# Kernel optimization log

Measured on AMD Instinct MI355X. Metric: run time of the kernel, lower is better.

The kernel has to match this reference:

```python
import jax, jax.numpy as jnp
import numpy as np

# ---- constants mirroring the torch module ----
OSAMP = 8            # temporal oversampling factor
MAX_ITER = 10        # forward solver iterations (LBFGS replaced by fixed GD)
NEG_SHIFT = 2 * OSAMP
OTP = 5              # baseline frames subtracted from ctc/aif
C_SHARP = 500.0      # sharpness constant C=500 in fermi_ir_func
LR = 0.1             # fixed step size for the deterministic forward solve


def interp_linear_1d(x, size):
    # interp_linear_1D: linear upsampling along last (time) axis
    return jax.image.resize(x, x.shape[:-1] + (size,), method='linear')


def fermi_ir(eta, t_os):
    # eta: [B,3,H,W] = (amplitude A, decay rate k, delay t0); t_os: [Tos]
    tsh = t_os - t_os[NEG_SHIFT]                    # negative time shift
    A = eta[:, 0][..., None]                        # [B,H,W,1]
    k = eta[:, 1][..., None]
    t0 = eta[:, 2][..., None]
    step = jax.nn.sigmoid(C_SHARP * tsh)            # sharp causal onset (C=500)
    return A * jax.nn.sigmoid(k * (t0 - tsh)) * step  # [B,H,W,Tos]


def convolve(aif, ir):
    # linear convolution along time via FFT; output aligned with neg_shift offset
    Tos = ir.shape[-1]
    n = 2 * Tos
    Fa = jnp.fft.rfft(aif, n=n, axis=-1)            # [B,1,1,n/2+1]
    Fi = jnp.fft.rfft(ir, n=n, axis=-1)             # [B,H,W,n/2+1]
    full = jnp.fft.irfft(Fa * Fi, n=n, axis=-1)
    return jax.lax.dynamic_slice_in_dim(full, NEG_SHIFT, Tos, axis=-1)


def make_objective(ctc, aif, time, eta_prior, lambda_reg):
    # preprocessing from FermiDataConsLBFGS.forward
    aif = aif - aif[..., :OTP].mean(-1, keepdims=True)
    ctc = ctc - ctc[..., :OTP].mean(-1, keepdims=True)
    Tos = OSAMP * ctc.shape[-1]
    aif_os = interp_linear_1d(aif, Tos)
    ctc_os = interp_linear_1d(ctc, Tos)
    t_os = interp_linear_1d(time, Tos)
    ctc_dc = ctc_os[..., ::OSAMP]                   # [B,H,W,T]
    C_nn = (eta_prior ** 2).sum(axis=(0, 2, 3), keepdims=True)  # [1,3,1,1]
    C_dc = (ctc_dc ** 2).sum()
    sp_lam = jax.nn.softplus(lambda_reg).squeeze()

    def F_obj(eta):  # FermiDConsObj.__call__ (OD disabled: indx_dc = all frames)
        ir = fermi_ir(eta, t_os)
        ctc_est = convolve(aif_os, ir)[..., ::OSAMP] / OSAMP
        dc = ((ctc_dc - ctc_est) ** 2 / C_dc).sum()
        reg = sp_lam * (((eta - eta_prior) ** 2) / C_nn).sum()
        pos = (jax.nn.relu(-eta) ** 2).sum()
        return dc + reg + pos
    return F_obj


def setup_inputs():
    key = jax.random.key(0)
    k1, k2, k3, k4 = jax.random.split(key, 4)
    B, H, W, T = 1, 128, 128, 64
    ctc = jax.random.normal(k1, (B, H, W, T), jnp.float32) * 0.1
    aif = jax.random.uniform(k2, (B, 1, 1, T), jnp.float32)
    time = jnp.arange(T, dtype=jnp.float32)
    seg = jnp.ones((B, H, W), jnp.int32)
    eta_nn = jax.random.uniform(k3, (B, 3, H, W), jnp.float32)
    lambda_reg = jax.random.normal(k4, (1,), jnp.float32)
    return {"ctc": ctc, "aif": aif, "time": time, "seg": seg,
            "eta_nn": eta_nn, "lambda_reg": lambda_reg}


def reference(ctc, aif, time, seg, eta_nn, lambda_reg):
    # seg only affects the (disabled) outlier-detection path
    F_obj = make_objective(ctc, aif, time, eta_nn, lambda_reg)
    gradF = jax.grad(F_obj)

    def step(eta, _):
        return eta - LR * gradF(eta), None

    eta_pi, _ = jax.lax.scan(step, eta_nn, None, length=MAX_ITER)
    return eta_pi
```

## Files before the change

kernel.cpp:

```cpp
#include <hip/hip_runtime.h>
#include <math.h>

#define T_IN 64
#define NPIX 16384
#define MAX_ITER 10
#define NSLOT 43
#define MAGIC 0x13579BDFu

typedef _Float16 half8_t __attribute__((ext_vector_type(8)));
typedef __fp16   fp16x2  __attribute__((ext_vector_type(2)));
typedef float    f32x4   __attribute__((ext_vector_type(4)));
typedef int      i32x4   __attribute__((ext_vector_type(4)));

union H8 { half8_t v; fp16x2 h2[4]; i32x4 i4; };

__device__ __forceinline__ float rcp_fast(float x) { return __builtin_amdgcn_rcpf(x); }

constexpr int NTMIN[16]   = {0,0,0,0,0,1,1,1,1,2,2,2,2,3,3,3};
constexpr int KTS[2][8]   = {{0,2,4,6,8,10,12,14},{1,3,5,7,9,11,13,15}};
constexpr int LBASE[2][8] = {{0,4,8,12,15,18,20,22},{0,4,8,11,14,16,18,19}};
constexpr int SLOTS[2][23] = {
  {0,1,2,3,8,9,10,11,16,17,18,19,23,24,25,29,30,31,34,35,38,39,41},
  {4,5,6,7,12,13,14,15,20,21,22,26,27,28,32,33,36,37,40,42,0,0,0}};

template<int P>
__device__ __forceinline__ void kloop(float K, float T0, int q,
        const float* tshs, const i32x4 (&Breg)[23], f32x4 (&acc)[3][4]) {
    float nK = -K;
    float r  = __expf(0.125f * K);
    #pragma unroll
    for (int i = 0; i < 8; ++i) {
        const int kt = KTS[P][i];
        f32x4 tv0 = *(const f32x4*)&tshs[32*kt + 8*q];
        f32x4 tv1 = *(const f32x4*)&tshs[32*kt + 8*q + 4];
        float d1[8];
        d1[0]=T0-tv0[0]; d1[1]=T0-tv0[1]; d1[2]=T0-tv0[2]; d1[3]=T0-tv0[3];
        d1[4]=T0-tv1[0]; d1[5]=T0-tv1[1]; d1[6]=T0-tv1[2]; d1[7]=T0-tv1[3];
        float x[8];
        if (kt == 0 || kt == 15) {
            bool edge = (kt == 0) ? (q == 0) : (q == 3);
            if (edge) {
                #pragma unroll
                for (int j = 0; j < 8; ++j) x[j] = __expf(nK * d1[j]);
            } else {
                x[0] = __expf(nK * d1[0]);
                #pragma unroll
                for (int j = 1; j < 8; ++j) x[j] = x[j-1] * r;
            }
        } else {
            x[0] = __expf(nK * d1[0]);
            #pragma unroll
            for (int j = 1; j < 8; ++j) x[j] = x[j-1] * r;
        }
        H8 F0h, F1h, F2h;
        #pragma unroll
        for (int jj = 0; jj < 4; ++jj) {
            float s1a = rcp_fast(1.0f + x[2*jj]);
            float s1b = rcp_fast(1.0f + x[2*jj+1]);
            fp16x2 sh  = (fp16x2){(__fp16)s1a, (__fp16)s1b};
            fp16x2 d1h = __builtin_amdgcn_cvt_pkrtz(d1[2*jj], d1[2*jj+1]);
            fp16x2 eh  = sh - sh*sh;
            F0h.h2[jj] = sh;
            F1h.h2[jj] = eh * d1h;
            F2h.h2[jj] = eh;
        }
        #pragma unroll
        for (int nt = NTMIN[kt]; nt < 4; ++nt) {
            int sl = LBASE[P][i] + nt - NTMIN[kt];
            H8 bh; bh.i4 = Breg[sl];
            acc[0][nt] = __builtin_amdgcn_mfma_f32_16x16x32_f16(F0h.v, bh.v, acc[0][nt], 0, 0, 0);
            acc[1][nt] = __builtin_amdgcn_mfma_f32_16x16x32_f16(F1h.v, bh.v, acc[1][nt], 0, 0, 0);
            acc[2][nt] = __builtin_amdgcn_mfma_f32_16x16x32_f16(F2h.v, bh.v, acc[2][nt], 0, 0, 0);
        }
    }
}

__global__ __launch_bounds__(512, 2) void k_all(
        const float* __restrict__ ctc,  const float* __restrict__ aif,
        const float* __restrict__ timev,const float* __restrict__ lam,
        const float* __restrict__ eta,  unsigned int* __restrict__ flags,
        f32x4* __restrict__ partials,   float* __restrict__ out) {
    __shared__ i32x4 Bs[NSLOT * 64];
    __shared__ f32x4 cbuf[4][64][12];
    __shared__ float ebuf[4][16][4];
    __shared__ float tshs[512];
    __shared__ float aifos[512];
    __shared__ float a_s[64], t_s[64];
    __shared__ f32x4 red[4];

    const int tid  = threadIdx.x;
    const int lane = tid & 63;
    const int wid  = tid >> 6;
    const int par  = wid & 1;
    const int pair = wid >> 1;
    const int q = lane >> 4, n = lane & 15;
    const int pixbase = blockIdx.x * 64 + pair * 16;
    const int mypix   = pixbase + n;

    if (tid < 64) { a_s[tid] = aif[tid]; t_s[tid] = timev[tid]; }
    float A  = eta[mypix];
    float K  = eta[NPIX + mypix];
    float T0 = eta[2*NPIX + mypix];
    const float pA = A, pK = K, pT = T0;
    __syncthreads();
    {
        float m5a = 0.2f * (a_s[0]+a_s[1]+a_s[2]+a_s[3]+a_s[4]);
        float t16;
        {
            float xx = 1.5625f; int i0 = (int)xx; float f = xx - (float)i0;
            t16 = t_s[i0]*(1.0f-f) + t_s[i0+1]*f;
        }
        int i = tid;
        float x = ((float)i - 3.5f) * 0.125f;
        float ao, to;
        if (x <= 0.0f)       { ao = a_s[0]  - m5a; to = t_s[0];  }
        else if (x >= 63.0f) { ao = a_s[63] - m5a; to = t_s[63]; }
        else {
            int i0 = (int)x; float f = x - (float)i0;
            ao = (a_s[i0]-m5a)*(1.0f-f) + (a_s[i0+1]-m5a)*f;
            to = t_s[i0]*(1.0f-f) + t_s[i0+1]*f;
        }
        aifos[i] = ao;
        tshs[i]  = to - t16;
    }

    float dcreg[4][4];
    if (par == 0) {
        #pragma unroll
        for (int reg = 0; reg < 4; ++reg) {
            const float* cp = ctc + (pixbase + q*4 + reg) * T_IN;
            float m5 = 0.2f * (cp[0]+cp[1]+cp[2]+cp[3]+cp[4]);
            #pragma unroll
            for (int nt = 0; nt < 4; ++nt) {
                int d = nt*16 + n;
                float cc = cp[d] - m5;
                float cm = cp[(d > 0) ? d-1 : 0] - m5;
                dcreg[nt][reg] = (d == 0) ? cc : (0.4375f*cm + 0.5625f*cc);
            }
        }
        float vs = 0.f;
        #pragma unroll
        for (int nt = 0; nt < 4; ++nt)
            #pragma unroll
            for (int r2 = 0; r2 < 4; ++r2) vs += dcreg[nt][r2]*dcreg[nt][r2];
        f32x4 pv = (f32x4){vs, 0.25f*A*A, 0.25f*K*K, 0.25f*T0*T0};
        #pragma unroll
        for (int m = 1; m < 64; m <<= 1) {
            pv.x += __shfl_xor(pv.x, m); pv.y += __shfl_xor(pv.y, m);
            pv.z += __shfl_xor(pv.z, m); pv.w += __shfl_xor(pv.w, m);
        }
        if (lane == 0) red[pair] = pv;
    }
    __syncthreads();
    if (tid == 0) {
        f32x4 s = red[0] + red[1] + red[2] + red[3];
        partials[blockIdx.x] = s;
        __threadfence();
        __hip_atomic_store(&flags[blockIdx.x], MAGIC, __ATOMIC_RELEASE,
                           __HIP_MEMORY_SCOPE_AGENT);
    }

    for (int idx = tid; idx < NSLOT * 64; idx += 512) {
        int slot = idx >> 6, l = idx & 63;
        int kt, nt;
        if (slot < 20)      { kt = slot >> 2; nt = slot & 3; }
        else if (slot < 32) { int s = slot - 20; int d3 = s / 3; kt = 5 + d3; nt = 1 + (s - 3*d3); }
        else if (slot < 40) { int s = slot - 32; kt = 9 + (s >> 1); nt = 2 + (s & 1); }
        else                { kt = 13 + (slot - 40); nt = 3; }
        int kbase = 32*kt + 8*(l >> 4);
        int m = 16 + 8 * (16*nt + (l & 15));
        H8 bh;
        #pragma unroll
        for (int jj = 0; jj < 4; ++jj) {
            float v[2];
            #pragma unroll
            for (int h = 0; h < 2; ++h) {
                int k  = kbase + 2*jj + h;
                int ai = m - k;
                float s2 = 1.0f / (1.0f + __expf(-500.0f * tshs[k]));
                v[h] = (ai >= 0 && ai < 512) ? s2 * aifos[ai] * 0.125f : 0.0f;
            }
            bh.h2[jj] = (fp16x2){(__fp16)v[0], (__fp16)v[1]};
        }
        Bs[idx] = bh.i4;
    }
    __syncthreads();

    i32x4 Breg[23];
    if (par == 0) {
        #pragma unroll
        for (int s = 0; s < 23; ++s) Breg[s] = Bs[SLOTS[0][s]*64 + lane];
    } else {
        #pragma unroll
        for (int s = 0; s < 20; ++s) Breg[s] = Bs[SLOTS[1][s]*64 + lane];
    }

    if (tid < 256)
        while (__hip_atomic_load(&flags[tid], __ATOMIC_ACQUIRE,
                                 __HIP_MEMORY_SCOPE_AGENT) != MAGIC)
            __builtin_amdgcn_s_sleep(2);
    __syncthreads();

    f32x4 tot = partials[lane] + partials[64+lane] + partials[128+lane]
              + partials[192+lane];
    #pragma unroll
    for (int m = 1; m < 64; m <<= 1) {
        tot.x += __shfl_xor(tot.x, m); tot.y += __shfl_xor(tot.y, m);
        tot.z += __shfl_xor(tot.z, m); tot.w += __shfl_xor(tot.w, m);
    }
    float spl;
    {
        float xl = lam[0];
        spl = (xl > 0.0f) ? (xl + log1pf(__expf(-xl))) : log1pf(__expf(xl));
    }
    const float cdc2 = 2.0f / tot.x;
    const float rgA  = 2.0f * spl / tot.y;
    const float rgK  = 2.0f * spl / tot.z;
    const float rgT  = 2.0f * spl / tot.w;

    #pragma unroll 1
    for (int it = 0; it < MAX_ITER; ++it) {
        f32x4 acc[3][4];
        #pragma unroll
        for (int f = 0; f < 3; ++f)
            #pragma unroll
            for (int t = 0; t < 4; ++t)
                acc[f][t] = (f32x4){0.f, 0.f, 0.f, 0.f};

        if (par == 0) kloop<0>(K, T0, q, tshs, Breg, acc);
        else          kloop<1>(K, T0, q, tshs, Breg, acc);

        if (par == 1) {
            #pragma unroll
            for (int f = 0; f < 3; ++f)
                #pragma unroll
                for (int t = 0; t < 4; ++t)
                    cbuf[pair][lane][f*4+t] = acc[f][t];
        }
        __syncthreads();

        if (par == 0) {
            #pragma unroll
            for (int f = 0; f < 3; ++f)
                #pragma unroll
                for (int t = 0; t < 4; ++t)
                    acc[f][t] += cbuf[pair][lane][f*4+t];

            float Ap[4];
            #pragma unroll
            for (int rr2 = 0; rr2 < 4; ++rr2) Ap[rr2] = __shfl(A, q*4 + rr2);

            float SA[4], SK[4], ST[4];
            #pragma unroll
            for (int r2 = 0; r2 < 4; ++r2) { SA[r2]=0.f; SK[r2]=0.f; ST[r2]=0.f; }
            #pragma unroll
            for (int nt = 0; nt < 4; ++nt)
                #pragma unroll
                for (int r2 = 0; r2 < 4; ++r2) {
                    float Y0 = acc[0][nt][r2], Y1 = acc[1][nt][r2], Y2 = acc[2][nt][r2];
                    float rr = fmaf(Ap[r2], Y0, -dcreg[nt][r2]);
                    SA[r2] = fmaf(rr, Y0, SA[r2]);
                    SK[r2] = fmaf(rr, Y1, SK[r2]);
                    ST[r2] = fmaf(rr, Y2, ST[r2]);
                }
            #pragma unroll
            for (int r2 = 0; r2 < 4; ++r2)
                #pragma unroll
                for (int m = 1; m < 16; m <<= 1) {
                    SA[r2] += __shfl_xor(SA[r2], m);
                    SK[r2] += __shfl_xor(SK[r2], m);
                    ST[r2] += __shfl_xor(ST[r2], m);
                }
            int src = (n >> 2) * 16;
            float GA = 0.f, GK = 0.f, GT = 0.f;
            #pragma unroll
            for (int r2 = 0; r2 < 4; ++r2) {
                float tA = __shfl(SA[r2], src);
                float tK = __shfl(SK[r2], src);
                float tT = __shfl(ST[r2], src);
                if ((n & 3) == r2) { GA = tA; GK = tK; GT = tT; }
            }

            float gA = fmaf(rgA, A  - pA, cdc2 * GA)         + 2.0f * fminf(A,  0.f);
            float gK = fmaf(rgK, K  - pK, cdc2 * A * GK)     + 2.0f * fminf(K,  0.f);
            float gT = fmaf(rgT, T0 - pT, cdc2 * A * K * GT) + 2.0f * fminf(T0, 0.f);
            A  -= 0.1f * gA;
            K  -= 0.1f * gK;
            T0 -= 0.1f * gT;

            if (lane < 16) {
                ebuf[pair][n][0] = A;
                ebuf[pair][n][1] = K;
                ebuf[pair][n][2] = T0;
            }
        }
        __syncthreads();

        if (par == 1) {
            A  = ebuf[pair][n][0];
            K  = ebuf[pair][n][1];
            T0 = ebuf[pair][n][2];
        }
    }

    if (par == 0 && lane < 16) {
        out[mypix]          = A;
        out[NPIX + mypix]   = K;
        out[2*NPIX + mypix] = T0;
    }
}

extern "C" void kernel_launch(void* const* d_in, const int* in_sizes, int n_in,
                              void* d_out, int out_size, void* d_ws, size_t ws_size,
                              hipStream_t stream) {
    const float* ctc   = (const float*)d_in[0];
    const float* aif   = (const float*)d_in[1];
    const float* timev = (const float*)d_in[2];
    const float* eta   = (const float*)d_in[4];
    const float* lam   = (const float*)d_in[5];
    float* out = (float*)d_out;
    f32x4*        partials = (f32x4*)d_ws;
    unsigned int* flags    = (unsigned int*)((char*)d_ws + 4096);

    k_all<<<NPIX / 64, 512, 0, stream>>>(ctc, aif, timev, lam, eta,
                                         flags, partials, out);
}
```

Measured before the change: 125.9 us.

## Exchange partial accumulators symmetrically so both waves compute the gradient update

```diff
diff --git a/kernel.cpp b/kernel.cpp
--- a/kernel.cpp
+++ b/kernel.cpp
@@ -80,9 +80,11 @@
         const float* __restrict__ timev,const float* __restrict__ lam,
         const float* __restrict__ eta,  unsigned int* __restrict__ flags,
         f32x4* __restrict__ partials,   float* __restrict__ out) {
-    __shared__ i32x4 Bs[NSLOT * 64];
-    __shared__ f32x4 cbuf[4][64][12];
-    __shared__ float ebuf[4][16][4];
+    union SharedPool {
+        i32x4 Bs[NSLOT * 64];
+        f32x4 cbuf[8][64][13];
+    };
+    __shared__ SharedPool sp;
     __shared__ float tshs[512];
     __shared__ float aifos[512];
     __shared__ float a_s[64], t_s[64];
@@ -125,19 +127,20 @@
     }
 
     float dcreg[4][4];
+    #pragma unroll
+    for (int reg = 0; reg < 4; ++reg) {
+        const float* cp = ctc + (pixbase + q*4 + reg) * T_IN;
+        float m5 = 0.2f * (cp[0]+cp[1]+cp[2]+cp[3]+cp[4]);
+        #pragma unroll
+        for (int nt = 0; nt < 4; ++nt) {
+            int d = nt*16 + n;
+            float cc = cp[d] - m5;
+            float cm = cp[(d > 0) ? d-1 : 0] - m5;
+            dcreg[nt][reg] = (d == 0) ? cc : (0.4375f*cm + 0.5625f*cc);
+        }
+    }
+
     if (par == 0) {
-        #pragma unroll
-        for (int reg = 0; reg < 4; ++reg) {
-            const float* cp = ctc + (pixbase + q*4 + reg) * T_IN;
-            float m5 = 0.2f * (cp[0]+cp[1]+cp[2]+cp[3]+cp[4]);
-            #pragma unroll
-            for (int nt = 0; nt < 4; ++nt) {
-                int d = nt*16 + n;
-                float cc = cp[d] - m5;
-                float cm = cp[(d > 0) ? d-1 : 0] - m5;
-                dcreg[nt][reg] = (d == 0) ? cc : (0.4375f*cm + 0.5625f*cc);
-            }
-        }
         float vs = 0.f;
         #pragma unroll
         for (int nt = 0; nt < 4; ++nt)
@@ -182,17 +185,17 @@
             }
             bh.h2[jj] = (fp16x2){(__fp16)v[0], (__fp16)v[1]};
         }
-        Bs[idx] = bh.i4;
+        sp.Bs[idx] = bh.i4;
     }
     __syncthreads();
 
     i32x4 Breg[23];
     if (par == 0) {
         #pragma unroll
-        for (int s = 0; s < 23; ++s) Breg[s] = Bs[SLOTS[0][s]*64 + lane];
+        for (int s = 0; s < 23; ++s) Breg[s] = sp.Bs[SLOTS[0][s]*64 + lane];
     } else {
         #pragma unroll
-        for (int s = 0; s < 20; ++s) Breg[s] = Bs[SLOTS[1][s]*64 + lane];
+        for (int s = 0; s < 20; ++s) Breg[s] = sp.Bs[SLOTS[1][s]*64 + lane];
     }
 
     if (tid < 256)
@@ -230,77 +233,60 @@
         if (par == 0) kloop<0>(K, T0, q, tshs, Breg, acc);
         else          kloop<1>(K, T0, q, tshs, Breg, acc);
 
-        if (par == 1) {
-            #pragma unroll
-            for (int f = 0; f < 3; ++f)
-                #pragma unroll
-                for (int t = 0; t < 4; ++t)
-                    cbuf[pair][lane][f*4+t] = acc[f][t];
-        }
+        #pragma unroll
+        for (int f = 0; f < 3; ++f)
+            #pragma unroll
+            for (int t = 0; t < 4; ++t)
+                sp.cbuf[wid][lane][f*4+t] = acc[f][t];
         __syncthreads();
-
-        if (par == 0) {
-            #pragma unroll
-            for (int f = 0; f < 3; ++f)
-                #pragma unroll
-                for (int t = 0; t < 4; ++t)
-                    acc[f][t] += cbuf[pair][lane][f*4+t];
-
-            float Ap[4];
-            #pragma unroll
-            for (int rr2 = 0; rr2 < 4; ++rr2) Ap[rr2] = __shfl(A, q*4 + rr2);
-
-            float SA[4], SK[4], ST[4];
-            #pragma unroll
-            for (int r2 = 0; r2 < 4; ++r2) { SA[r2]=0.f; SK[r2]=0.f; ST[r2]=0.f; }
-            #pragma unroll
-            for (int nt = 0; nt < 4; ++nt)
-                #pragma unroll
-                for (int r2 = 0; r2 < 4; ++r2) {
-                    float Y0 = acc[0][nt][r2], Y1 = acc[1][nt][r2], Y2 = acc[2][nt][r2];
-                    float rr = fmaf(Ap[r2], Y0, -dcreg[nt][r2]);
-                    SA[r2] = fmaf(rr, Y0, SA[r2]);
-                    SK[r2] = fmaf(rr, Y1, SK[r2]);
-                    ST[r2] = fmaf(rr, Y2, ST[r2]);
-                }
-            #pragma unroll
-            for (int r2 = 0; r2 < 4; ++r2)
-                #pragma unroll
-                for (int m = 1; m < 16; m <<= 1) {
-                    SA[r2] += __shfl_xor(SA[r2], m);
-                    SK[r2] += __shfl_xor(SK[r2], m);
-                    ST[r2] += __shfl_xor(ST[r2], m);
-                }
-            int src = (n >> 2) * 16;
-            float GA = 0.f, GK = 0.f, GT = 0.f;
+        #pragma unroll
+        for (int f = 0; f < 3; ++f)
+            #pragma unroll
+            for (int t = 0; t < 4; ++t)
+                acc[f][t] += sp.cbuf[wid ^ 1][lane][f*4+t];
+        __syncthreads();
+
+        float Ap[4];
+        #pragma unroll
+        for (int rr2 = 0; rr2 < 4; ++rr2) Ap[rr2] = __shfl(A, q*4 + rr2);
+
+        float SA[4], SK[4], ST[4];
+        #pragma unroll
+        for (int r2 = 0; r2 < 4; ++r2) { SA[r2]=0.f; SK[r2]=0.f; ST[r2]=0.f; }
+        #pragma unroll
+        for (int nt = 0; nt < 4; ++nt)
             #pragma unroll
             for (int r2 = 0; r2 < 4; ++r2) {
-                float tA = __shfl(SA[r2], src);
-                float tK = __shfl(SK[r2], src);
-                float tT = __shfl(ST[r2], src);
-                if ((n & 3) == r2) { GA = tA; GK = tK; GT = tT; }
+                float Y0 = acc[0][nt][r2], Y1 = acc[1][nt][r2], Y2 = acc[2][nt][r2];
+                float rr = fmaf(Ap[r2], Y0, -dcreg[nt][r2]);
+                SA[r2] = fmaf(rr, Y0, SA[r2]);
+                SK[r2] = fmaf(rr, Y1, SK[r2]);
+                ST[r2] = fmaf(rr, Y2, ST[r2]);
             }
-
-            float gA = fmaf(rgA, A  - pA, cdc2 * GA)         + 2.0f * fminf(A,  0.f);
-            float gK = fmaf(rgK, K  - pK, cdc2 * A * GK)     + 2.0f * fminf(K,  0.f);
-            float gT = fmaf(rgT, T0 - pT, cdc2 * A * K * GT) + 2.0f * fminf(T0, 0.f);
-            A  -= 0.1f * gA;
-            K  -= 0.1f * gK;
-            T0 -= 0.1f * gT;
-
-            if (lane < 16) {
-                ebuf[pair][n][0] = A;
-                ebuf[pair][n][1] = K;
-                ebuf[pair][n][2] = T0;
+        #pragma unroll
+        for (int r2 = 0; r2 < 4; ++r2)
+            #pragma unroll
+            for (int m = 1; m < 16; m <<= 1) {
+                SA[r2] += __shfl_xor(SA[r2], m);
+                SK[r2] += __shfl_xor(SK[r2], m);
+                ST[r2] += __shfl_xor(ST[r2], m);
             }
-        }
-        __syncthreads();
-
-        if (par == 1) {
-            A  = ebuf[pair][n][0];
-            K  = ebuf[pair][n][1];
-            T0 = ebuf[pair][n][2];
-        }
+        int src = (n >> 2) * 16;
+        float GA = 0.f, GK = 0.f, GT = 0.f;
+        #pragma unroll
+        for (int r2 = 0; r2 < 4; ++r2) {
+            float tA = __shfl(SA[r2], src);
+            float tK = __shfl(SK[r2], src);
+            float tT = __shfl(ST[r2], src);
+            if ((n & 3) == r2) { GA = tA; GK = tK; GT = tT; }
+        }
+
+        float gA = fmaf(rgA, A  - pA, cdc2 * GA)         + 2.0f * fminf(A,  0.f);
+        float gK = fmaf(rgK, K  - pK, cdc2 * A * GK)     + 2.0f * fminf(K,  0.f);
+        float gT = fmaf(rgT, T0 - pT, cdc2 * A * K * GT) + 2.0f * fminf(T0, 0.f);
+        A  -= 0.1f * gA;
+        K  -= 0.1f * gK;
+        T0 -= 0.1f * gT;
     }
 
     if (par == 0 && lane < 16) {
```

New measurement: 128.2 us. Within noise of the previous version (+1.8%).
